# Kernel optimization log

Hardware: AMD Instinct MI355X
Metric: run time of the kernel (lower is better)

## Reference

```python
import jax, jax.numpy as jnp
import numpy as np

T = 33554432


def setup_inputs() -> dict:
    # Original module computes this internally: betas = linspace(1e-4, 0.02, T).
    # We materialize it here as the single input so the op is exercised on real data.
    betas = jnp.linspace(1e-4, 0.02, T, dtype=jnp.float32)
    return {"betas": betas}


def reference(betas):
    # alphas = 1 - betas ; alpha_bars[i] = prod(alphas[:i+1])  (O(T) cumprod,
    # replacing the original O(T^2) Python loop of torch.prod over prefixes)
    alphas = 1.0 - betas
    alpha_bars = jnp.cumprod(alphas)
    return alpha_bars
```

## Files before the change

### kernel.cpp

```cpp
#include <hip/hip_runtime.h>


typedef float f32x4 __attribute__((ext_vector_type(4)));

#define BLOCK 256
#define EPB   (BLOCK * 4)
#define SEQ   32

__global__ __launch_bounds__(BLOCK) void k_block_prod(const float* __restrict__ betas,
                                                      float* __restrict__ bp, int n) {
    const int tid  = threadIdx.x;
    const int bid  = blockIdx.x;
    const long i4  = ((long)bid * BLOCK + tid) * 4;

    float a[4] = {1.0f, 1.0f, 1.0f, 1.0f};
    if (i4 + 4 <= n) {
        f32x4 b = *reinterpret_cast<const f32x4*>(betas + i4);
        a[0] = 1.0f - b.x; a[1] = 1.0f - b.y; a[2] = 1.0f - b.z; a[3] = 1.0f - b.w;
    } else {
#pragma unroll
        for (int k = 0; k < 4; ++k) {
            long i = i4 + k;
            if (i < n) a[k] = 1.0f - betas[i];
        }
    }
    float t = (a[0] * a[1]) * (a[2] * a[3]);

#pragma unroll
    for (int off = 1; off < 64; off <<= 1) t *= __shfl_xor(t, off, 64);

    __shared__ float w[BLOCK / 64];
    const int lane = tid & 63, wid = tid >> 6;
    if (lane == 0) w[wid] = t;
    __syncthreads();
    if (tid == 0) bp[bid] = (w[0] * w[1]) * (w[2] * w[3]);
}

__global__ __launch_bounds__(1024) void k_scan_bp(const float* __restrict__ bp,
                                                  float* __restrict__ excl, int nb) {
    const int tid  = threadIdx.x;
    const int base = tid * SEQ;
    const int lane = tid & 63, wid = tid >> 6;

    float v[SEQ];
    float t = 1.0f;
#pragma unroll
    for (int k = 0; k < SEQ; ++k) {
        float x = (base + k < nb) ? bp[base + k] : 1.0f;
        v[k] = x;
        t *= x;
    }

    float incl = t;
#pragma unroll
    for (int off = 1; off < 64; off <<= 1) {
        float u = __shfl_up(incl, off, 64);
        if (lane >= off) incl *= u;
    }

    __shared__ float wtot[1024 / 64];
    if (lane == 63) wtot[wid] = incl;
    __syncthreads();

    float wexcl = 1.0f;
    for (int q = 0; q < wid; ++q) wexcl *= wtot[q];

    float texcl = __shfl_up(incl, 1, 64);
    if (lane == 0) texcl = 1.0f;

    float run = wexcl * texcl;
#pragma unroll
    for (int k = 0; k < SEQ; ++k) {
        if (base + k < nb) excl[base + k] = run;
        run *= v[k];
    }
}

__global__ __launch_bounds__(BLOCK) void k_final(const float* __restrict__ betas,
                                                 const float* __restrict__ excl,
                                                 float* __restrict__ out, int n) {
    const int tid = threadIdx.x;
    const int bid = blockIdx.x;
    const long i4 = ((long)bid * BLOCK + tid) * 4;
    const bool full = (i4 + 4 <= n);

    __shared__ float s_carry;
    if (tid == 0) s_carry = excl[bid];
    __syncthreads();
    const float carry = s_carry;

    if (carry == 0.0f) {
        if (full) {
            f32x4 z = {0.0f, 0.0f, 0.0f, 0.0f};
            __builtin_nontemporal_store(z, reinterpret_cast<f32x4*>(out + i4));
        } else {
            for (int k = 0; k < 4; ++k) {
                long i = i4 + k;
                if (i < n) out[i] = 0.0f;
            }
        }
        return;
    }

    float a[4] = {1.0f, 1.0f, 1.0f, 1.0f};
    if (full) {
        f32x4 b = *reinterpret_cast<const f32x4*>(betas + i4);
        a[0] = 1.0f - b.x; a[1] = 1.0f - b.y; a[2] = 1.0f - b.z; a[3] = 1.0f - b.w;
    } else {
#pragma unroll
        for (int k = 0; k < 4; ++k) {
            long i = i4 + k;
            if (i < n) a[k] = 1.0f - betas[i];
        }
    }

    float r0 = a[0];
    float r1 = r0 * a[1];
    float r2 = r1 * a[2];
    float r3 = r2 * a[3];

    const int lane = tid & 63, wid = tid >> 6;
    float incl = r3;
#pragma unroll
    for (int off = 1; off < 64; off <<= 1) {
        float u = __shfl_up(incl, off, 64);
        if (lane >= off) incl *= u;
    }

    __shared__ float wtot[BLOCK / 64];
    if (lane == 63) wtot[wid] = incl;
    __syncthreads();

    float wexcl = 1.0f;
#pragma unroll
    for (int q = 0; q < BLOCK / 64; ++q)
        if (q < wid) wexcl *= wtot[q];

    float texcl = __shfl_up(incl, 1, 64);
    if (lane == 0) texcl = 1.0f;

    const float p = carry * wexcl * texcl;

    if (full) {
        f32x4 o;
        o.x = p * r0; o.y = p * r1; o.z = p * r2; o.w = p * r3;
        __builtin_nontemporal_store(o, reinterpret_cast<f32x4*>(out + i4));
    } else {
#pragma unroll
        for (int k = 0; k < 4; ++k) {
            long i = i4 + k;
            if (i < n) {
                float r = (k == 0) ? r0 : (k == 1) ? r1 : (k == 2) ? r2 : r3;
                out[i] = p * r;
            }
        }
    }
}

extern "C" void kernel_launch(void* const* d_in, const int* in_sizes, int n_in,
                              void* d_out, int out_size, void* d_ws, size_t ws_size,
                              hipStream_t stream) {
    const float* betas = (const float*)d_in[0];
    float* out = (float*)d_out;
    const int n  = in_sizes[0];
    const int nb = (n + EPB - 1) / EPB;

    float* bp   = (float*)d_ws;
    float* excl = bp + nb;

    k_block_prod<<<nb, BLOCK, 0, stream>>>(betas, bp, n);
    k_scan_bp<<<1, 1024, 0, stream>>>(bp, excl, nb);
    k_final<<<nb, BLOCK, 0, stream>>>(betas, excl, out, n);
}
```

Measured before the change: 253.3 us.

## Split block-product scan into head and tail, skipping tail once product underflows

Computes block products and their scan only for the first 2048 tiles. If the running product has already reached zero, it writes a flag, zero-fills the remaining carries and skips the tail block-product and tail scan kernels. This avoids reading the bulk of betas in the first pass when the cumulative product underflows. It adds two kernel launches and a serial dependency, and the tail path runs only when there is no underflow.

```diff
diff --git a/kernel.cpp b/kernel.cpp
--- a/kernel.cpp
+++ b/kernel.cpp
@@ -4,14 +4,16 @@
 typedef float f32x4 __attribute__((ext_vector_type(4)));
 
 #define BLOCK 256
-#define EPB   (BLOCK * 4)
-#define SEQ   32
-
-__global__ __launch_bounds__(BLOCK) void k_block_prod(const float* __restrict__ betas,
-                                                      float* __restrict__ bp, int n) {
-    const int tid  = threadIdx.x;
-    const int bid  = blockIdx.x;
-    const long i4  = ((long)bid * BLOCK + tid) * 4;
+#define EPB   1024
+#define HEAD  2048
+#define SEQ_H 2
+#define SEQ_T 30
+
+__global__ __launch_bounds__(BLOCK) void k1_head_bp(const float* __restrict__ betas,
+                                                    float* __restrict__ bp, int n) {
+    const int tid = threadIdx.x;
+    const int bid = blockIdx.x;
+    const long i4 = ((long)bid * BLOCK + tid) * 4;
 
     float a[4] = {1.0f, 1.0f, 1.0f, 1.0f};
     if (i4 + 4 <= n) {
@@ -19,13 +21,9 @@
         a[0] = 1.0f - b.x; a[1] = 1.0f - b.y; a[2] = 1.0f - b.z; a[3] = 1.0f - b.w;
     } else {
 #pragma unroll
-        for (int k = 0; k < 4; ++k) {
-            long i = i4 + k;
-            if (i < n) a[k] = 1.0f - betas[i];
-        }
+        for (int k = 0; k < 4; ++k) { long i = i4 + k; if (i < n) a[k] = 1.0f - betas[i]; }
     }
     float t = (a[0] * a[1]) * (a[2] * a[3]);
-
 #pragma unroll
     for (int off = 1; off < 64; off <<= 1) t *= __shfl_xor(t, off, 64);
 
@@ -36,19 +34,20 @@
     if (tid == 0) bp[bid] = (w[0] * w[1]) * (w[2] * w[3]);
 }
 
-__global__ __launch_bounds__(1024) void k_scan_bp(const float* __restrict__ bp,
-                                                  float* __restrict__ excl, int nb) {
+__global__ __launch_bounds__(1024) void k2_head_scan(const float* __restrict__ bp,
+                                                     float* __restrict__ excl,
+                                                     int* __restrict__ zflag, int nb) {
     const int tid  = threadIdx.x;
-    const int base = tid * SEQ;
-    const int lane = tid & 63, wid = tid >> 6;
-
-    float v[SEQ];
+    const int base = tid * SEQ_H;
+    const int lane = tid & 63, wid = tid >> 6;
+    const int hb   = (nb < HEAD) ? nb : HEAD;
+
+    float v[SEQ_H];
     float t = 1.0f;
 #pragma unroll
-    for (int k = 0; k < SEQ; ++k) {
-        float x = (base + k < nb) ? bp[base + k] : 1.0f;
-        v[k] = x;
-        t *= x;
+    for (int k = 0; k < SEQ_H; ++k) {
+        float x = (base + k < hb) ? bp[base + k] : 1.0f;
+        v[k] = x; t *= x;
     }
 
     float incl = t;
@@ -63,22 +62,114 @@
     __syncthreads();
 
     float wexcl = 1.0f;
-    for (int q = 0; q < wid; ++q) wexcl *= wtot[q];
+#pragma unroll
+    for (int q = 0; q < 1024 / 64; ++q) if (q < wid) wexcl *= wtot[q];
 
     float texcl = __shfl_up(incl, 1, 64);
     if (lane == 0) texcl = 1.0f;
 
     float run = wexcl * texcl;
 #pragma unroll
-    for (int k = 0; k < SEQ; ++k) {
+    for (int k = 0; k < SEQ_H; ++k) {
+        if (base + k < hb) excl[base + k] = run;
+        run *= v[k];
+    }
+
+    __shared__ int s_zf;
+    if (tid == 1023) {
+        int zf = (run == 0.0f) ? 1 : 0;
+        s_zf = zf;
+        *zflag = zf;
+    }
+    __syncthreads();
+
+    if (s_zf) {
+        for (int j = HEAD + tid; j < nb; j += 1024) excl[j] = 0.0f;
+    }
+}
+
+__global__ __launch_bounds__(BLOCK) void k3_tail_bp(const float* __restrict__ betas,
+                                                    float* __restrict__ bp,
+                                                    const int* __restrict__ zflag,
+                                                    int n, int nb) {
+    __shared__ int s_zf;
+    if (threadIdx.x == 0) s_zf = *zflag;
+    __syncthreads();
+    if (s_zf) return;
+
+    const int tid = threadIdx.x;
+    const int lane = tid & 63, wid = tid >> 6;
+    __shared__ float w[BLOCK / 64];
+
+    for (int tile = HEAD + blockIdx.x; tile < nb; tile += gridDim.x) {
+        const long i4 = ((long)tile * EPB) + (long)tid * 4;
+        float a[4] = {1.0f, 1.0f, 1.0f, 1.0f};
+        if (i4 + 4 <= n) {
+            f32x4 b = *reinterpret_cast<const f32x4*>(betas + i4);
+            a[0] = 1.0f - b.x; a[1] = 1.0f - b.y; a[2] = 1.0f - b.z; a[3] = 1.0f - b.w;
+        } else {
+#pragma unroll
+            for (int k = 0; k < 4; ++k) { long i = i4 + k; if (i < n) a[k] = 1.0f - betas[i]; }
+        }
+        float t = (a[0] * a[1]) * (a[2] * a[3]);
+#pragma unroll
+        for (int off = 1; off < 64; off <<= 1) t *= __shfl_xor(t, off, 64);
+        if (lane == 0) w[wid] = t;
+        __syncthreads();
+        if (tid == 0) bp[tile] = (w[0] * w[1]) * (w[2] * w[3]);
+        __syncthreads();
+    }
+}
+
+__global__ __launch_bounds__(1024) void k4_tail_scan(const float* __restrict__ bp,
+                                                     float* __restrict__ excl,
+                                                     const int* __restrict__ zflag, int nb) {
+    if (*zflag) return;
+    if (nb <= HEAD) return;
+
+    const int tid  = threadIdx.x;
+    const int base = HEAD + tid * SEQ_T;
+    const int lane = tid & 63, wid = tid >> 6;
+
+    const float seed = excl[HEAD - 1] * bp[HEAD - 1];
+
+    float v[SEQ_T];
+    float t = 1.0f;
+#pragma unroll
+    for (int k = 0; k < SEQ_T; ++k) {
+        float x = (base + k < nb) ? bp[base + k] : 1.0f;
+        v[k] = x; t *= x;
+    }
+
+    float incl = t;
+#pragma unroll
+    for (int off = 1; off < 64; off <<= 1) {
+        float u = __shfl_up(incl, off, 64);
+        if (lane >= off) incl *= u;
+    }
+
+    __shared__ float wtot[1024 / 64];
+    if (lane == 63) wtot[wid] = incl;
+    __syncthreads();
+
+    float wexcl = 1.0f;
+#pragma unroll
+    for (int q = 0; q < 1024 / 64; ++q) if (q < wid) wexcl *= wtot[q];
+
+    float texcl = __shfl_up(incl, 1, 64);
+    if (lane == 0) texcl = 1.0f;
+
+    float run = seed * wexcl * texcl;
+#pragma unroll
+    for (int k = 0; k < SEQ_T; ++k) {
         if (base + k < nb) excl[base + k] = run;
         run *= v[k];
     }
 }
 
-__global__ __launch_bounds__(BLOCK) void k_final(const float* __restrict__ betas,
-                                                 const float* __restrict__ excl,
-                                                 float* __restrict__ out, int n) {
+__global__ __launch_bounds__(BLOCK) void k5_final(const float* __restrict__ betas,
+                                                  const float* __restrict__ excl,
+                                                  float* __restrict__ out, int n) {
     const int tid = threadIdx.x;
     const int bid = blockIdx.x;
     const long i4 = ((long)bid * BLOCK + tid) * 4;
@@ -94,10 +185,7 @@
             f32x4 z = {0.0f, 0.0f, 0.0f, 0.0f};
             __builtin_nontemporal_store(z, reinterpret_cast<f32x4*>(out + i4));
         } else {
-            for (int k = 0; k < 4; ++k) {
-                long i = i4 + k;
-                if (i < n) out[i] = 0.0f;
-            }
+            for (int k = 0; k < 4; ++k) { long i = i4 + k; if (i < n) out[i] = 0.0f; }
         }
         return;
     }
@@ -108,10 +196,7 @@
         a[0] = 1.0f - b.x; a[1] = 1.0f - b.y; a[2] = 1.0f - b.z; a[3] = 1.0f - b.w;
     } else {
 #pragma unroll
-        for (int k = 0; k < 4; ++k) {
-            long i = i4 + k;
-            if (i < n) a[k] = 1.0f - betas[i];
-        }
+        for (int k = 0; k < 4; ++k) { long i = i4 + k; if (i < n) a[k] = 1.0f - betas[i]; }
     }
 
     float r0 = a[0];
@@ -133,8 +218,7 @@
 
     float wexcl = 1.0f;
 #pragma unroll
-    for (int q = 0; q < BLOCK / 64; ++q)
-        if (q < wid) wexcl *= wtot[q];
+    for (int q = 0; q < BLOCK / 64; ++q) if (q < wid) wexcl *= wtot[q];
 
     float texcl = __shfl_up(incl, 1, 64);
     if (lane == 0) texcl = 1.0f;
@@ -165,10 +249,15 @@
     const int n  = in_sizes[0];
     const int nb = (n + EPB - 1) / EPB;
 
-    float* bp   = (float*)d_ws;
-    float* excl = bp + nb;
-
-    k_block_prod<<<nb, BLOCK, 0, stream>>>(betas, bp, n);
-    k_scan_bp<<<1, 1024, 0, stream>>>(bp, excl, nb);
-    k_final<<<nb, BLOCK, 0, stream>>>(betas, excl, out, n);
-}
+    float* bp    = (float*)d_ws;
+    float* excl  = bp + nb;
+    int*   zflag = (int*)(excl + nb);
+
+    const int g1 = (nb < HEAD) ? nb : HEAD;
+
+    k1_head_bp  <<<g1,   BLOCK, 0, stream>>>(betas, bp, n);
+    k2_head_scan<<<1,    1024,  0, stream>>>(bp, excl, zflag, nb);
+    k3_tail_bp  <<<2048, BLOCK, 0, stream>>>(betas, bp, zflag, n, nb);
+    k4_tail_scan<<<1,    1024,  0, stream>>>(bp, excl, zflag, nb);
+    k5_final    <<<nb,   BLOCK, 0, stream>>>(betas, excl, out, n);
+}
```

Result: faster. 206.7 us (-18.4%).
